# Performance work log

Hardware: AMD Instinct MI355X
Metric: run time of the kernel (lower is better)

## Reference

```python
import jax, jax.numpy as jnp
import numpy as np

N_NODES = 50000
N_EDGES = 800000
IN_F = 128
OUT_F = 32
HEADS = 4
EDGE_DIM = 8
ALPHA = 0.2  # LeakyReLU negative slope


def setup_inputs() -> dict:
    key = jax.random.key(0)
    k0, k1, k2, k3, k4 = jax.random.split(key, 5)
    x = jax.random.normal(k0, (N_NODES, IN_F), dtype=jnp.float32)
    edge_index = jax.random.randint(k1, (2, N_EDGES), 0, N_NODES, dtype=jnp.int32)
    edge_attr = jax.random.normal(k2, (N_EDGES, EDGE_DIM), dtype=jnp.float32)
    # xavier-ish init for parameters
    W = jax.random.normal(k3, (HEADS, IN_F, OUT_F), dtype=jnp.float32) * (1.0 / np.float32(np.sqrt(IN_F)))
    a = jax.random.normal(k4, (HEADS, 2 * OUT_F + EDGE_DIM, 1), dtype=jnp.float32) * np.float32(0.1)
    return {"x": x, "edge_index": edge_index, "edge_attr": edge_attr, "W": W, "a": a}


def reference(x, edge_index, edge_attr, W, a):
    n_nodes = x.shape[0]
    out_f = W.shape[2]
    src, dst = edge_index[0], edge_index[1]

    # per-head linear transform: (N, H, O)
    xt = jnp.einsum('ni,hio->nho', x, W)
    x_src = xt[src]  # (E, H, O) edge gather
    x_dst = xt[dst]  # (E, H, O)

    # split attention vector a = [a_src | a_dst | a_edge]; equivalent to
    # einsum('ehi,hio->eho', cat([x_src, x_dst, edge]), a) without the concat
    av = a[..., 0]                      # (H, 2O+D)
    a_s = av[:, :out_f]                 # (H, O)
    a_d = av[:, out_f:2 * out_f]        # (H, O)
    a_e = av[:, 2 * out_f:]             # (H, D)
    e = (jnp.einsum('eho,ho->eh', x_src, a_s)
         + jnp.einsum('eho,ho->eh', x_dst, a_d)
         + edge_attr @ a_e.T)           # (E, H)
    e = jnp.where(e > 0, e, ALPHA * e)  # LeakyReLU

    # segment (per-destination) softmax over incoming edges, per head
    max_e = jax.ops.segment_max(e, dst, num_segments=n_nodes)   # (N, H), -inf on empty
    max_e = jnp.where(jnp.isneginf(max_e), jnp.zeros_like(max_e), max_e)
    exp_e = jnp.exp(e - max_e[dst])                             # (E, H)
    sum_exp = jax.ops.segment_sum(exp_e, dst, num_segments=n_nodes)  # (N, H)
    attention = exp_e / (sum_exp[dst] + 1e-10)                  # (E, H)

    # weighted scatter-add aggregation
    weighted = x_src * attention[:, :, None]                    # (E, H, O)
    out = jax.ops.segment_sum(weighted, dst, num_segments=n_nodes)  # (N, H, O)
    return out.reshape(n_nodes, -1)  # concat=True -> (N, H*O)
```

## Files before the change

### kernel.cpp

```cpp
#include <hip/hip_runtime.h>
#include <hip/hip_fp16.h>

#define N_NODES 50000
#define N_EDGES 800000
#define IN_F    128
#define OUT_F   32
#define HEADS   4
#define EDGE_DIM 8
#define LRELU_ALPHA 0.2f

#define EPB 2048
#define BT  1024
#define EPT (EPB / BT)
#define NBUCK 98
#define NBLK_A ((N_EDGES + EPB - 1) / EPB)
#define NODES_PER_BUCK 512
#define CAP 10240

typedef float    floatx4 __attribute__((ext_vector_type(4)));
typedef unsigned uintx4  __attribute__((ext_vector_type(4)));
typedef short    short4v __attribute__((ext_vector_type(4)));
typedef short    short8v __attribute__((ext_vector_type(8)));
typedef float    f32x4   __attribute__((ext_vector_type(4)));

__device__ __forceinline__ unsigned f2bf(float f) {
  unsigned u = __float_as_uint(f);
  return (u + 0x7fffu + ((u >> 16) & 1u)) >> 16;
}

__global__ __launch_bounds__(128) void k_wprep(
    const float* __restrict__ W, unsigned short* __restrict__ wtg,
    unsigned* __restrict__ bfill) {
  const int row = blockIdx.x;
  const int i = threadIdx.x;
  if (row == 0 && i < NBUCK) bfill[i] = (unsigned)(i * CAP);
  const float v = W[(row >> 5) * (IN_F * OUT_F) + i * OUT_F + (row & 31)];
  wtg[row * 128 + i] = (unsigned short)f2bf(v);
}

__global__ __launch_bounds__(256) void k_transform(
    const float* __restrict__ x, const unsigned short* __restrict__ wtg,
    const float* __restrict__ a, unsigned* __restrict__ xtb,
    float* __restrict__ alpha_src, float* __restrict__ alpha_dst) {
  __shared__ short sxb[64][138];
  __shared__ short wt[128][132];
  const int t = threadIdx.x;
  const int n0 = blockIdx.x * 64;

#pragma unroll
  for (int r = 0; r < 8; ++r) {
    const int f = r * 256 + t;
    const int row = f >> 4;
    const int c8 = (f & 15) * 8;
    const short8v v =
        *reinterpret_cast<const short8v*>(&wtg[row * 128 + c8]);
    *reinterpret_cast<short8v*>(&wt[row][c8]) = v;
  }

#pragma unroll
  for (int r = 0; r < 8; ++r) {
    const int f = r * 256 + t;
    const int node = f >> 5;
    const int i4 = (f & 31) * 4;
    const int n = n0 + node;
    float4 v = make_float4(0.f, 0.f, 0.f, 0.f);
    if (n < N_NODES) v = *reinterpret_cast<const float4*>(&x[(size_t)n * 128 + i4]);
    short4v s4;
    s4.x = (short)f2bf(v.x);
    s4.y = (short)f2bf(v.y);
    s4.z = (short)f2bf(v.z);
    s4.w = (short)f2bf(v.w);
    *reinterpret_cast<short4v*>(&sxb[node][i4]) = s4;
  }
  __syncthreads();

  const int w = t >> 6;
  const int lane = t & 63;
  const int r16 = lane & 15;
  const int kg = lane >> 4;

  f32x4 acc[8];
#pragma unroll
  for (int nt = 0; nt < 8; ++nt) acc[nt] = (f32x4)(0.f);

#pragma unroll
  for (int kk = 0; kk < 4; ++kk) {
    const short8v afrag =
        *reinterpret_cast<const short8v*>(&sxb[w * 16 + r16][kk * 32 + kg * 8]);
#pragma unroll
    for (int nt = 0; nt < 8; ++nt) {
      const short8v bfrag =
          *reinterpret_cast<const short8v*>(&wt[nt * 16 + r16][kk * 32 + kg * 8]);
      acc[nt] = __builtin_amdgcn_mfma_f32_16x16x32_bf16(afrag, bfrag, acc[nt],
                                                        0, 0, 0);
    }
  }

  __syncthreads();
  unsigned* __restrict__ xp = reinterpret_cast<unsigned*>(&wt[0][0]);

#pragma unroll
  for (int nt = 0; nt < 8; ++nt) {
#pragma unroll
    for (int reg = 0; reg < 4; ++reg) {
      const float v = acc[nt][reg];
      const float vp = __shfl_xor(v, 1, 64);
      if (!(lane & 1)) {
        const int nodeL = w * 16 + kg * 4 + reg;
        const int node = n0 + nodeL;
        const unsigned u = f2bf(v) | (f2bf(vp) << 16);
        xp[nodeL * 66 + nt * 8 + (r16 >> 1)] = u;
        if (node < N_NODES) {
          xtb[(size_t)node * 64 + nt * 8 + (r16 >> 1)] = u;
        }
      }
    }
  }
  __syncthreads();

  {
    const int nodeL = t >> 2;
    const int q = t & 3;
    const int node = n0 + nodeL;
    if (node < N_NODES) {
      const unsigned* __restrict__ row = &xp[nodeL * 66 + q * 16];
      const float* __restrict__ as = &a[q * 72];
      const float* __restrict__ ad = &a[q * 72 + 32];
      float s = 0.f, d = 0.f;
#pragma unroll
      for (int j = 0; j < 16; ++j) {
        const unsigned u = row[j];
        const float lo = __uint_as_float(u << 16);
        const float hi = __uint_as_float(u & 0xffff0000u);
        s = fmaf(lo, as[2 * j], s);
        s = fmaf(hi, as[2 * j + 1], s);
        d = fmaf(lo, ad[2 * j], d);
        d = fmaf(hi, ad[2 * j + 1], d);
      }
      alpha_src[node * 4 + q] = s;
      alpha_dst[node * 4 + q] = d;
    }
  }
}

__device__ __forceinline__ uintx4 make_entry(
    int e, int src, int dst, const float* __restrict__ ea,
    const float* __restrict__ a, const float* __restrict__ alpha_src,
    const float* __restrict__ alpha_dst) {
  const floatx4 ev0 = __builtin_nontemporal_load(
      reinterpret_cast<const floatx4*>(&ea[(size_t)e * EDGE_DIM]));
  const floatx4 ev1 = __builtin_nontemporal_load(
      reinterpret_cast<const floatx4*>(&ea[(size_t)e * EDGE_DIM + 4]));
  const float4 als = *reinterpret_cast<const float4*>(&alpha_src[src * 4]);
  const float4 ald = *reinterpret_cast<const float4*>(&alpha_dst[dst * 4]);
  const float* alsp = reinterpret_cast<const float*>(&als);
  const float* aldp = reinterpret_cast<const float*>(&ald);
  unsigned sh[4];
#pragma unroll
  for (int h = 0; h < HEADS; ++h) {
    float s = alsp[h] + aldp[h];
    const float* ae = &a[h * 72 + 64];
    s = fmaf(ev0.x, ae[0], s);
    s = fmaf(ev0.y, ae[1], s);
    s = fmaf(ev0.z, ae[2], s);
    s = fmaf(ev0.w, ae[3], s);
    s = fmaf(ev1.x, ae[4], s);
    s = fmaf(ev1.y, ae[5], s);
    s = fmaf(ev1.z, ae[6], s);
    s = fmaf(ev1.w, ae[7], s);
    s = s > 0.f ? s : LRELU_ALPHA * s;
    sh[h] = (unsigned)__half_as_ushort(__float2half(s));
  }
  uintx4 ent;
  ent.x = (unsigned)src;
  ent.y = sh[0] | (sh[1] << 16);
  ent.z = sh[2] | (sh[3] << 16);
  ent.w = (unsigned)dst;
  return ent;
}

__global__ __launch_bounds__(BT) void k_binsort(
    const int* __restrict__ ei, const float* __restrict__ ea,
    const float* __restrict__ a, const float* __restrict__ alpha_src,
    const float* __restrict__ alpha_dst, unsigned* __restrict__ bfill,
    uintx4* __restrict__ stage) {
  __shared__ uintx4 sent[EPB];
  __shared__ unsigned lhist[128];
  __shared__ unsigned lscan[128];
  __shared__ unsigned gb[128];
  const int t = threadIdx.x;
  const int e0 = blockIdx.x * EPB;
  const int nvalid = min(EPB, N_EDGES - e0);

  if (t < 128) lhist[t] = 0u;
  __syncthreads();

  uintx4 ent[EPT];
  int bk[EPT];
  int lpos[EPT];
#pragma unroll
  for (int k = 0; k < EPT; ++k) {
    const int e = e0 + k * BT + t;
    bk[k] = -1;
    if (e < N_EDGES) {
      const int src = __builtin_nontemporal_load(&ei[e]);
      const int dst = __builtin_nontemporal_load(&ei[N_EDGES + e]);
      ent[k] = make_entry(e, src, dst, ea, a, alpha_src, alpha_dst);
      bk[k] = dst >> 9;
      lpos[k] = (int)atomicAdd(&lhist[bk[k]], 1u);
    }
  }
  __syncthreads();

  if (t < 128) lscan[t] = lhist[t];
  __syncthreads();
#pragma unroll
  for (int off = 1; off < 128; off <<= 1) {
    unsigned v = 0u;
    if (t < 128 && t >= off) v = lscan[t - off];
    __syncthreads();
    if (t < 128) lscan[t] += v;
    __syncthreads();
  }
  if (t < NBUCK) {
    const unsigned cnt = lhist[t];
    lscan[t] -= cnt;
    gb[t] = cnt ? atomicAdd(&bfill[t], cnt) : 0u;
  }
  __syncthreads();

#pragma unroll
  for (int k = 0; k < EPT; ++k) {
    if (bk[k] >= 0) {
      const int p = (int)lscan[bk[k]] + lpos[k];
      sent[p] = ent[k];
    }
  }
  __syncthreads();

#pragma unroll
  for (int k = 0; k < EPT; ++k) {
    const int p = k * BT + t;
    if (p < nvalid) {
      const uintx4 sv = sent[p];
      const int b = (int)(sv.w >> 9);
      stage[gb[b] + (unsigned)(p - (int)lscan[b])] = sv;
    }
  }
}

__global__ __launch_bounds__(1024) void k_place(
    const unsigned* __restrict__ bfill, const uintx4* __restrict__ stage,
    unsigned* __restrict__ rs, uintx4* __restrict__ csr) {
  __shared__ unsigned lbuf[NODES_PER_BUCK];
  __shared__ unsigned wsum[8];
  __shared__ unsigned bscan[128];
  const int b = blockIdx.x;
  const int t = threadIdx.x;
  const int node0 = b << 9;
  const int nn = min(NODES_PER_BUCK, N_NODES - node0);
  const unsigned base = (unsigned)(b * CAP);

  if (t < 128) {
    bscan[t] = (t < NBUCK) ? (bfill[t] - (unsigned)(t * CAP)) : 0u;
  }
  __syncthreads();
#pragma unroll
  for (int off = 1; off < 128; off <<= 1) {
    unsigned v = 0u;
    if (t < 128 && t >= off) v = bscan[t - off];
    __syncthreads();
    if (t < 128) bscan[t] += v;
    __syncthreads();
  }
  const unsigned cnt = bfill[b] - base;
  const unsigned bs = (b == 0) ? 0u : bscan[b - 1];

  if (t < NODES_PER_BUCK) lbuf[t] = 0u;
  __syncthreads();

  for (unsigned i = t; i < cnt; i += 1024) {
    const unsigned dst = __builtin_nontemporal_load(&stage[base + i]).w;
    atomicAdd(&lbuf[dst - (unsigned)node0], 1u);
  }
  __syncthreads();

  const unsigned c = (t < NODES_PER_BUCK) ? lbuf[t] : 0u;
  unsigned incl = c;
  const int lane = t & 63;
#pragma unroll
  for (int off = 1; off < 64; off <<= 1) {
    const unsigned n = __shfl_up(incl, off, 64);
    if (lane >= off) incl += n;
  }
  if (t < NODES_PER_BUCK && lane == 63) wsum[t >> 6] = incl;
  __syncthreads();
  if (t < 8) {
    const unsigned wv = wsum[t];
    unsigned wincl = wv;
#pragma unroll
    for (int off = 1; off < 8; off <<= 1) {
      const unsigned n = __shfl_up(wincl, off, 64);
      if (t >= off) wincl += n;
    }
    wsum[t] = wincl - wv;
  }
  __syncthreads();
  if (t < NODES_PER_BUCK) {
    const unsigned excl = incl - c + wsum[t >> 6];
    lbuf[t] = bs + excl;
    if (t < nn) rs[node0 + t] = bs + excl;
  }
  if (b == NBUCK - 1 && t == 0) rs[N_NODES] = N_EDGES;
  __syncthreads();

  for (unsigned i = t; i < cnt; i += 1024) {
    const uintx4 ent = __builtin_nontemporal_load(&stage[base + i]);
    const unsigned slot = atomicAdd(&lbuf[ent.w - (unsigned)node0], 1u);
    csr[slot] = ent;
  }
}

__device__ __forceinline__ float ent_score(const uintx4& ent, int h) {
  const unsigned uu = (h < 2) ? ent.y : ent.z;
  const unsigned us = (h & 1) ? (uu >> 16) : (uu & 0xffffu);
  return __half2float(__ushort_as_half((unsigned short)us));
}

__global__ __launch_bounds__(256) void k_agg(
    const unsigned* __restrict__ rs, const uintx4* __restrict__ csr,
    const unsigned* __restrict__ xtb, float* __restrict__ out) {
  const int lane = threadIdx.x & 63;
  const int dst = (int)((blockIdx.x * (unsigned)blockDim.x + threadIdx.x) >> 6);
  if (dst >= N_NODES) return;

  const unsigned j0 = rs[dst];
  const unsigned j1 = rs[dst + 1];
  const int deg = (int)(j1 - j0);

  float a0 = 0.f, a1 = 0.f, lsum = 0.f;

  if (deg > 0) {
    const int rounds = (deg + 15) >> 4;
    const int eL = lane & 15;
    const int hB = lane >> 4;

    const uintx4 pad = {0u, 0xfc00fc00u, 0xfc00fc00u, 0u};

    for (int r = 0; r < rounds; ++r) {
      const int j = (int)j0 + r * 16 + eL;
      const uintx4 ent =
          (j < (int)j1) ? __builtin_nontemporal_load(&csr[j]) : pad;
      const float w = __expf(ent_score(ent, hB));
      lsum += w;
      const int sx = (int)ent.x;

      int ssrc[16];
#pragma unroll
      for (int jj = 0; jj < 16; ++jj)
        ssrc[jj] = __builtin_amdgcn_readlane(sx, jj);
      unsigned ud[16];
#pragma unroll
      for (int jj = 0; jj < 16; ++jj)
        ud[jj] = xtb[(size_t)ssrc[jj] * 64 + lane];
#define AGG_STEP(JJ)                                                         \
  {                                                                          \
    const float wj = __int_as_float(__builtin_amdgcn_ds_swizzle(             \
        __float_as_int(w), ((JJ) << 5) | 0x10));                             \
    a0 = fmaf(wj, __uint_as_float(ud[JJ] << 16), a0);                        \
    a1 = fmaf(wj, __uint_as_float(ud[JJ] & 0xffff0000u), a1);                \
  }
      AGG_STEP(0)  AGG_STEP(1)  AGG_STEP(2)  AGG_STEP(3)
      AGG_STEP(4)  AGG_STEP(5)  AGG_STEP(6)  AGG_STEP(7)
      AGG_STEP(8)  AGG_STEP(9)  AGG_STEP(10) AGG_STEP(11)
      AGG_STEP(12) AGG_STEP(13) AGG_STEP(14) AGG_STEP(15)
#undef AGG_STEP
    }
    lsum += __shfl_xor(lsum, 1, 64);
    lsum += __shfl_xor(lsum, 2, 64);
    lsum += __shfl_xor(lsum, 4, 64);
    lsum += __shfl_xor(lsum, 8, 64);
  }

  const float inv = 1.0f / (lsum + 1e-10f);
  __builtin_nontemporal_store(a0 * inv, &out[(size_t)dst * 128 + lane * 2 + 0]);
  __builtin_nontemporal_store(a1 * inv, &out[(size_t)dst * 128 + lane * 2 + 1]);
}

extern "C" void kernel_launch(void* const* d_in, const int* in_sizes, int n_in,
                              void* d_out, int out_size, void* d_ws,
                              size_t ws_size, hipStream_t stream) {
  const float* x = (const float*)d_in[0];
  const int* ei = (const int*)d_in[1];
  const float* ea = (const float*)d_in[2];
  const float* W = (const float*)d_in[3];
  const float* a = (const float*)d_in[4];
  float* out = (float*)d_out;

  char* p = (char*)d_ws;
  unsigned* xtb = (unsigned*)p;     p += (size_t)N_NODES * 64 * 4;
  uintx4* csr = (uintx4*)p;         p += (size_t)N_EDGES * 16;
  uintx4* stage = (uintx4*)p;       p += (size_t)NBUCK * CAP * 16;
  float* alpha_src = (float*)p;     p += (size_t)N_NODES * 4 * 4;
  float* alpha_dst = (float*)p;     p += (size_t)N_NODES * 4 * 4;
  unsigned* rs = (unsigned*)p;      p += (size_t)(N_NODES + 1) * 4;
  unsigned* bfill = (unsigned*)p;   p += 128 * 4;
  unsigned short* wtg = (unsigned short*)p; p += 128 * 128 * 2;

  k_wprep<<<128, 128, 0, stream>>>(W, wtg, bfill);
  k_transform<<<(N_NODES + 63) / 64, 256, 0, stream>>>(x, wtg, a, xtb,
                                                       alpha_src, alpha_dst);
  k_binsort<<<NBLK_A, BT, 0, stream>>>(ei, ea, a, alpha_src, alpha_dst, bfill,
                                       stage);
  k_place<<<NBUCK, 1024, 0, stream>>>(bfill, stage, rs, csr);
  k_agg<<<(N_NODES * 64 + 255) / 256, 256, 0, stream>>>(rs, csr, xtb, out);
}
```

Baseline: 109.3 us.

## Split aggregation into one wavefront per destination-head pair

The aggregation kernel now launches one wavefront per (head, destination) pair instead of one per destination. Each wavefront loads up to 64 edges at once and processes four edges in parallel across lane groups, with 16 lanes covering a head's 32 features. Partial sums are reduced with cross-group shuffles at the end. This quadruples the wavefront count to raise parallelism and spread edge latency, at the cost of reloading each destination's CSR entries once per head, narrower 64-byte gathers, and extra shuffle reductions.

```diff
diff --git a/kernel.cpp b/kernel.cpp
--- a/kernel.cpp
+++ b/kernel.cpp
@@ -331,60 +331,59 @@
     const unsigned* __restrict__ rs, const uintx4* __restrict__ csr,
     const unsigned* __restrict__ xtb, float* __restrict__ out) {
   const int lane = threadIdx.x & 63;
-  const int dst = (int)((blockIdx.x * (unsigned)blockDim.x + threadIdx.x) >> 6);
-  if (dst >= N_NODES) return;
+  const int gw = (int)((blockIdx.x * (unsigned)blockDim.x + threadIdx.x) >> 6);
+  const int h = gw / N_NODES;
+  const int dst = gw - h * N_NODES;
 
   const unsigned j0 = rs[dst];
   const unsigned j1 = rs[dst + 1];
   const int deg = (int)(j1 - j0);
 
+  const int eg = lane >> 4;
+  const int fp = lane & 15;
+
   float a0 = 0.f, a1 = 0.f, lsum = 0.f;
 
   if (deg > 0) {
-    const int rounds = (deg + 15) >> 4;
-    const int eL = lane & 15;
-    const int hB = lane >> 4;
-
     const uintx4 pad = {0u, 0xfc00fc00u, 0xfc00fc00u, 0u};
-
-    for (int r = 0; r < rounds; ++r) {
-      const int j = (int)j0 + r * 16 + eL;
+    const unsigned* __restrict__ xh = xtb + h * 16;
+
+    for (int r = 0; r < deg; r += 64) {
+      const int j = (int)j0 + r + lane;
       const uintx4 ent =
           (j < (int)j1) ? __builtin_nontemporal_load(&csr[j]) : pad;
-      const float w = __expf(ent_score(ent, hB));
+      const float w = __expf(ent_score(ent, h));
       lsum += w;
       const int sx = (int)ent.x;
 
-      int ssrc[16];
-#pragma unroll
-      for (int jj = 0; jj < 16; ++jj)
-        ssrc[jj] = __builtin_amdgcn_readlane(sx, jj);
-      unsigned ud[16];
-#pragma unroll
-      for (int jj = 0; jj < 16; ++jj)
-        ud[jj] = xtb[(size_t)ssrc[jj] * 64 + lane];
-#define AGG_STEP(JJ)                                                         \
-  {                                                                          \
-    const float wj = __int_as_float(__builtin_amdgcn_ds_swizzle(             \
-        __float_as_int(w), ((JJ) << 5) | 0x10));                             \
-    a0 = fmaf(wj, __uint_as_float(ud[JJ] << 16), a0);                        \
-    a1 = fmaf(wj, __uint_as_float(ud[JJ] & 0xffff0000u), a1);                \
-  }
-      AGG_STEP(0)  AGG_STEP(1)  AGG_STEP(2)  AGG_STEP(3)
-      AGG_STEP(4)  AGG_STEP(5)  AGG_STEP(6)  AGG_STEP(7)
-      AGG_STEP(8)  AGG_STEP(9)  AGG_STEP(10) AGG_STEP(11)
-      AGG_STEP(12) AGG_STEP(13) AGG_STEP(14) AGG_STEP(15)
-#undef AGG_STEP
-    }
+      const int nsub = min(16, (deg - r + 3) >> 2);
+      for (int s = 0; s < nsub; ++s) {
+        const int eidx = s * 4 + eg;
+        const int srcv = __shfl(sx, eidx, 64);
+        const float wv = __shfl(w, eidx, 64);
+        const unsigned u = xh[(size_t)srcv * 64 + fp];
+        a0 = fmaf(wv, __uint_as_float(u << 16), a0);
+        a1 = fmaf(wv, __uint_as_float(u & 0xffff0000u), a1);
+      }
+    }
+    a0 += __shfl_xor(a0, 16, 64);
+    a0 += __shfl_xor(a0, 32, 64);
+    a1 += __shfl_xor(a1, 16, 64);
+    a1 += __shfl_xor(a1, 32, 64);
     lsum += __shfl_xor(lsum, 1, 64);
     lsum += __shfl_xor(lsum, 2, 64);
     lsum += __shfl_xor(lsum, 4, 64);
     lsum += __shfl_xor(lsum, 8, 64);
-  }
-
-  const float inv = 1.0f / (lsum + 1e-10f);
-  __builtin_nontemporal_store(a0 * inv, &out[(size_t)dst * 128 + lane * 2 + 0]);
-  __builtin_nontemporal_store(a1 * inv, &out[(size_t)dst * 128 + lane * 2 + 1]);
+    lsum += __shfl_xor(lsum, 16, 64);
+    lsum += __shfl_xor(lsum, 32, 64);
+  }
+
+  if (eg == 0) {
+    const float inv = 1.0f / (lsum + 1e-10f);
+    float* __restrict__ op = &out[(size_t)dst * 128 + h * 32 + fp * 2];
+    __builtin_nontemporal_store(a0 * inv, op);
+    __builtin_nontemporal_store(a1 * inv, op + 1);
+  }
 }
 
 extern "C" void kernel_launch(void* const* d_in, const int* in_sizes, int n_in,
@@ -413,5 +412,5 @@
   k_binsort<<<NBLK_A, BT, 0, stream>>>(ei, ea, a, alpha_src, alpha_dst, bfill,
                                        stage);
   k_place<<<NBUCK, 1024, 0, stream>>>(bfill, stage, rs, csr);
-  k_agg<<<(N_NODES * 64 + 255) / 256, 256, 0, stream>>>(rs, csr, xtb, out);
-}
+  k_agg<<<(N_NODES * HEADS * 64) / 256, 256, 0, stream>>>(rs, csr, xtb, out);
+}
```

After: 172.3 us. 57.6% more time.
